# Performance work log

Measured on AMD Instinct MI355X. Metric: run time of the kernel, lower is better.

The kernel has to match this reference:

```python
import jax, jax.numpy as jnp
import numpy as np

DIM = 256
N_EMBED = 1024
COMMITMENT_COST = 0.25


def setup_inputs() -> dict:
    key = jax.random.key(0)
    k1, k2 = jax.random.split(key)
    z = jax.random.normal(k1, (16, 256, 64, 64), dtype=jnp.float32)
    # nn.Embedding weight initialized uniform(-1/n_embed, 1/n_embed)
    embed = jax.random.uniform(k2, (N_EMBED, DIM), dtype=jnp.float32,
                               minval=-1.0 / N_EMBED, maxval=1.0 / N_EMBED)
    return {"z": z, "embed": embed}


def reference(z, embed):
    sg = jax.lax.stop_gradient
    # NCHW -> NHWC, flatten spatial+batch to tokens
    zp = jnp.transpose(z, (0, 2, 3, 1))            # [B,H,W,C]
    zf = zp.reshape(-1, DIM)                        # [N, C]
    # squared euclidean distances via expansion: |z|^2 + |e|^2 - 2 z.e
    d = (jnp.sum(zf * zf, axis=1, keepdims=True)
         + jnp.sum(embed * embed, axis=1)
         - 2.0 * zf @ embed.T)                      # [N, K]
    idx = jnp.argmin(d, axis=1)                     # [N]
    min_encodings = jax.nn.one_hot(idx, N_EMBED, dtype=zf.dtype)  # [N, K]
    # direct gather == one-hot @ embed (same math, one HBM pass)
    z_q = embed[idx].reshape(zp.shape)              # [B,H,W,C]
    loss = (jnp.mean((sg(z_q) - zp) ** 2)
            + COMMITMENT_COST * jnp.mean((z_q - sg(zp)) ** 2))
    # straight-through estimator
    z_q_st = zp + sg(z_q - zp)
    e_mean = jnp.mean(min_encodings, axis=0)
    perplexity = jnp.exp(-jnp.sum(e_mean * jnp.log(e_mean + 1e-10)))
    z_q_out = jnp.transpose(z_q_st, (0, 3, 1, 2))   # back to NCHW
    return (loss, z_q_out, perplexity, min_encodings, idx[:, None])
```

## Files before the change

### kernel.cpp

```cpp
#include <hip/hip_runtime.h>
#include <math.h>

#define DIM    256
#define K_EMB  1024
#define HW     4096
#define CHW    1048576
#define N_TOK  65536
#define NELEM  16777216

#define OUT_LOSS 0
#define OUT_ZQ   1
#define OUT_PERP 16777217
#define OUT_MENC 16777218LL
#define OUT_IDX  83886082

#define TAU  1.5e-4f
#define CAND_CAP 16

#define TAIL_ROW0  65407
#define EH_OFF     66976770LL

typedef short short8  __attribute__((ext_vector_type(8)));
typedef float floatx4 __attribute__((ext_vector_type(4)));
typedef float floatx2 __attribute__((ext_vector_type(2)));

__device__ __forceinline__ unsigned short f2bf(float f) {
    unsigned int u = __float_as_uint(f);
    return (unsigned short)((u + 0x7FFFu + ((u >> 16) & 1u)) >> 16);
}
__device__ __forceinline__ float bf2f(unsigned short h) {
    return __uint_as_float(((unsigned int)h) << 16);
}

__device__ __forceinline__ float np_pair128(const float* p) {
    float r[8];
    #pragma unroll
    for (int j = 0; j < 8; ++j) r[j] = p[j];
    for (int i = 8; i < 128; i += 8)
        #pragma unroll
        for (int j = 0; j < 8; ++j) r[j] = __fadd_rn(r[j], p[i + j]);
    return __fadd_rn(__fadd_rn(__fadd_rn(r[0], r[1]), __fadd_rn(r[2], r[3])),
                     __fadd_rn(__fadd_rn(r[4], r[5]), __fadd_rn(r[6], r[7])));
}
__device__ __forceinline__ float np_pair256(const float* p) {
    return __fadd_rn(np_pair128(p), np_pair128(p + 128));
}

__device__ __forceinline__ void build_frags(const float* __restrict__ zp, int quad, short8* a) {
    #pragma unroll
    for (int kc = 0; kc < 8; ++kc) {
        short8 vh, vl;
        #pragma unroll
        for (int u = 0; u < 8; ++u) {
            float v = __builtin_nontemporal_load(zp + (size_t)(kc * 32 + quad * 8 + u) * HW);
            unsigned short h = f2bf(v);
            vh[u] = (short)h;
            vl[u] = (short)f2bf(v - bf2f(h));
        }
        a[kc]     = vh;
        a[8 + kc] = vl;
    }
}

__global__ void t2_np_kernel(const float* __restrict__ embed, float* __restrict__ t2,
                             unsigned short* __restrict__ Eh) {
    int k = blockIdx.x * 256 + threadIdx.x;
    if (k >= K_EMB) return;
    const float* e = embed + (size_t)k * DIM;
    float p[256];
    for (int c = 0; c < DIM; c += 4) {
        float4 v = *(const float4*)(e + c);
        p[c]     = __fmul_rn(v.x, v.x);
        p[c + 1] = __fmul_rn(v.y, v.y);
        p[c + 2] = __fmul_rn(v.z, v.z);
        p[c + 3] = __fmul_rn(v.w, v.w);
    }
    t2[k] = np_pair256(p);
    unsigned short* dst = Eh + (size_t)k * DIM;
    for (int c0 = 0; c0 < DIM; c0 += 8) {
        short8 vh;
        #pragma unroll
        for (int u = 0; u < 8; ++u) vh[u] = (short)f2bf(e[c0 + u]);
        *(short8*)(dst + c0) = vh;
    }
}

__launch_bounds__(256, 4)
__global__ void vq_mfma(const float* __restrict__ z,
                        const float* __restrict__ embed,
                        const unsigned short* __restrict__ Eh,
                        const float* __restrict__ t2g,
                        float* __restrict__ out,
                        unsigned int* __restrict__ counts,
                        float* __restrict__ loss_sum) {
    __shared__ unsigned short lds_b[32 * 264];
    __shared__ float t2_lds[K_EMB];
    __shared__ int midx[64];
    __shared__ unsigned short clist[64][CAND_CAP];
    __shared__ int ccnt[64];
    __shared__ int flist[64];
    __shared__ int fn;
    __shared__ float pp4[4][256];

    const int tid  = threadIdx.x;
    const int lane = tid & 63;
    const int wv   = tid >> 6;
    const int l15  = lane & 15;
    const int quad = lane >> 4;
    const int m0   = blockIdx.x * 64;

    for (int i = tid; i < K_EMB; i += 256) t2_lds[i] = t2g[i];
    if (tid < 64) ccnt[tid] = 0;
    if (tid == 0) fn = 0;

    short8 a[16];
    {
        const int n = m0 + wv * 16 + l15;
        build_frags(z + (size_t)(n >> 12) * CHW + (n & 4095), quad, a);
    }

    float bs[4], ss[4], tb[4]; int bk[4];
    #pragma unroll
    for (int r = 0; r < 4; ++r) { bs[r] = 3.4e38f; ss[r] = 3.4e38f; tb[r] = 3.4e38f; bk[r] = 0; }

    const int srow = tid >> 3;
    const int scol = (tid & 7) * 32;

    for (int it = 0; it < 32; ++it) {
        const int n0 = it * 32;
        __syncthreads();
        {
            const short8* g = (const short8*)(Eh + (size_t)(n0 + srow) * 256 + scol);
            short8* l = (short8*)(lds_b + srow * 264 + scol);
            short8 v0 = g[0], v1 = g[1], v2 = g[2], v3 = g[3];
            l[0] = v0; l[1] = v1; l[2] = v2; l[3] = v3;
        }
        __syncthreads();
        floatx4 acc0 = {0.f, 0.f, 0.f, 0.f};
        floatx4 acc1 = {0.f, 0.f, 0.f, 0.f};
        #pragma unroll
        for (int kc = 0; kc < 8; ++kc) {
            short8 b0 = *(const short8*)(lds_b + l15 * 264 + kc * 32 + quad * 8);
            short8 b1 = *(const short8*)(lds_b + (16 + l15) * 264 + kc * 32 + quad * 8);
            acc0 = __builtin_amdgcn_mfma_f32_16x16x32_bf16(a[kc],     b0, acc0, 0, 0, 0);
            acc1 = __builtin_amdgcn_mfma_f32_16x16x32_bf16(a[kc],     b1, acc1, 0, 0, 0);
            acc0 = __builtin_amdgcn_mfma_f32_16x16x32_bf16(a[8 + kc], b0, acc0, 0, 0, 0);
            acc1 = __builtin_amdgcn_mfma_f32_16x16x32_bf16(a[8 + kc], b1, acc1, 0, 0, 0);
        }
        float t20 = t2_lds[n0 + l15];
        float t21 = t2_lds[n0 + 16 + l15];
        #pragma unroll
        for (int r = 0; r < 4; ++r) {
            const int trow = wv * 16 + quad * 4 + r;
            float s0 = fmaf(-2.0f, acc0[r], t20);
            if (s0 < bs[r]) { ss[r] = bs[r]; bs[r] = s0; bk[r] = n0 + l15; }
            else if (s0 < ss[r]) ss[r] = s0;
            float s1 = fmaf(-2.0f, acc1[r], t21);
            if (s1 < bs[r]) { ss[r] = bs[r]; bs[r] = s1; bk[r] = n0 + 16 + l15; }
            else if (s1 < ss[r]) ss[r] = s1;

            float m01 = fminf(s0, s1);
            #pragma unroll
            for (int mo = 1; mo < 16; mo <<= 1) m01 = fminf(m01, __shfl_xor(m01, mo, 64));
            tb[r] = fminf(tb[r], m01);
            const float thr = tb[r] + TAU;
            if (s0 <= thr) {
                int pos = atomicAdd(&ccnt[trow], 1);
                if (pos < CAND_CAP) clist[trow][pos] = (unsigned short)(n0 + l15);
            }
            if (s1 <= thr) {
                int pos = atomicAdd(&ccnt[trow], 1);
                if (pos < CAND_CAP) clist[trow][pos] = (unsigned short)(n0 + 16 + l15);
            }
        }
    }

    #pragma unroll
    for (int r = 0; r < 4; ++r) {
        for (int mo = 1; mo < 16; mo <<= 1) {
            float obs = __shfl_xor(bs[r], mo, 64);
            float oss = __shfl_xor(ss[r], mo, 64);
            int   obk = __shfl_xor(bk[r], mo, 64);
            if (obs < bs[r] || (obs == bs[r] && obk < bk[r])) {
                ss[r] = fminf(bs[r], oss); bs[r] = obs; bk[r] = obk;
            } else {
                ss[r] = fminf(ss[r], obs);
            }
        }
        if (l15 == 0) {
            int tl = wv * 16 + quad * 4 + r;
            midx[tl] = bk[r];
            if (ss[r] - bs[r] < TAU) {
                int p = atomicAdd(&fn, 1);
                flist[p] = tl;
            }
        }
    }
    __syncthreads();

    const int nfb = fn;
    for (int f = wv; f < nfb; f += 4) {
        const int tl = flist[f];
        const int n  = m0 + tl;
        const int cnt = ccnt[tl];

        const float* zt = z + (size_t)(n >> 12) * CHW + (n & 4095);
        double zd[4];
        #pragma unroll
        for (int u = 0; u < 4; ++u) {
            float v = zt[(size_t)(lane + u * 64) * HW];
            zd[u] = (double)v;
            pp4[wv][lane + u * 64] = __fmul_rn(v, v);
        }
        __asm__ volatile("s_waitcnt lgkmcnt(0)" ::: "memory");
        float rj = 0.0f;
        if (lane < 16) {
            int jj = lane & 7, half = lane >> 3;
            const float* p = &pp4[wv][half * 128 + jj];
            rj = p[0];
            #pragma unroll
            for (int ii = 1; ii < 16; ++ii) rj = __fadd_rn(rj, p[ii * 8]);
        }
        float v0 = __shfl(rj, 0, 64), v1 = __shfl(rj, 1, 64), v2 = __shfl(rj, 2, 64), v3 = __shfl(rj, 3, 64);
        float v4 = __shfl(rj, 4, 64), v5 = __shfl(rj, 5, 64), v6 = __shfl(rj, 6, 64), v7 = __shfl(rj, 7, 64);
        float h0 = __fadd_rn(__fadd_rn(__fadd_rn(v0, v1), __fadd_rn(v2, v3)),
                             __fadd_rn(__fadd_rn(v4, v5), __fadd_rn(v6, v7)));
        v0 = __shfl(rj,  8, 64); v1 = __shfl(rj,  9, 64); v2 = __shfl(rj, 10, 64); v3 = __shfl(rj, 11, 64);
        v4 = __shfl(rj, 12, 64); v5 = __shfl(rj, 13, 64); v6 = __shfl(rj, 14, 64); v7 = __shfl(rj, 15, 64);
        float h1 = __fadd_rn(__fadd_rn(__fadd_rn(v0, v1), __fadd_rn(v2, v3)),
                             __fadd_rn(__fadd_rn(v4, v5), __fadd_rn(v6, v7)));
        const float t1 = __fadd_rn(h0, h1);

        float bd = 3.4e38f; int bkk = 1 << 30;
        if (cnt <= CAND_CAP) {
            for (int ci = 0; ci < cnt; ++ci) {
                int k = clist[tl][ci];
                const float* e = embed + (size_t)k * DIM;
                double s = 0.0;
                #pragma unroll
                for (int u = 0; u < 4; ++u) s = fma(zd[u], (double)e[lane + u * 64], s);
                for (int mo = 1; mo < 64; mo <<= 1) s += __shfl_xor(s, mo, 64);
                float rho = (float)s;
                float d = __fadd_rn(__fadd_rn(t1, t2_lds[k]), -__fmul_rn(2.0f, rho));
                if (d < bd || (d == bd && k < bkk)) { bd = d; bkk = k; }
            }
        } else {
            for (int k = 0; k < K_EMB; ++k) {
                const float* e = embed + (size_t)k * DIM;
                double s = 0.0;
                #pragma unroll
                for (int u = 0; u < 4; ++u) s = fma(zd[u], (double)e[lane + u * 64], s);
                for (int mo = 1; mo < 64; mo <<= 1) s += __shfl_xor(s, mo, 64);
                float rho = (float)s;
                float d = __fadd_rn(__fadd_rn(t1, t2_lds[k]), -__fmul_rn(2.0f, rho));
                if (d < bd) { bd = d; bkk = k; }
            }
        }
        if (lane == 0) midx[tl] = bkk;
    }
    __syncthreads();

    if (tid < 64) {
        const int id = midx[tid];
        out[OUT_IDX + m0 + tid] = (float)id;
        atomicAdd(&counts[id], 1u);
    }

    {
        const int n   = m0 + wv * 16 + l15;
        const int myk = midx[wv * 16 + l15];
        const float* erow = embed + (size_t)myk * DIM;
        float* zqp = out + OUT_ZQ + (size_t)(n >> 12) * CHW + (n & 4095);
        float lsum = 0.0f;
        #pragma unroll
        for (int kc = 0; kc < 8; ++kc) {
            const int c0 = kc * 32 + quad * 8;
            float4 e0 = *(const float4*)(erow + c0);
            float4 e1 = *(const float4*)(erow + c0 + 4);
            float ev[8] = {e0.x, e0.y, e0.z, e0.w, e1.x, e1.y, e1.z, e1.w};
            #pragma unroll
            for (int u = 0; u < 8; ++u) {
                float vv = __fadd_rn(bf2f((unsigned short)a[kc][u]),
                                     bf2f((unsigned short)a[8 + kc][u]));
                float dz = ev[u] - vv;
                lsum = fmaf(dz, dz, lsum);
                __builtin_nontemporal_store(ev[u], zqp + (size_t)(c0 + u) * HW);
            }
        }
        #pragma unroll
        for (int off = 32; off > 0; off >>= 1) lsum += __shfl_down(lsum, off, 64);
        if (lane == 0) atomicAdd(loss_sum, lsum);
    }

    #pragma unroll 1
    for (int j = 0; j < 64; ++j) {
        if (m0 + j >= TAIL_ROW0) break;
        const int id = midx[j];
        floatx2* dst = (floatx2*)(out + OUT_MENC + (size_t)(m0 + j) * K_EMB);
        int c0 = tid * 2;
        floatx2 v;  v.x  = (c0 == id)       ? 1.0f : 0.0f;  v.y  = (c0 + 1 == id)  ? 1.0f : 0.0f;
        __builtin_nontemporal_store(v, dst + tid);
        int c1 = c0 + 512;
        floatx2 w2; w2.x = (c1 == id)       ? 1.0f : 0.0f;  w2.y = (c1 + 1 == id)  ? 1.0f : 0.0f;
        __builtin_nontemporal_store(w2, dst + 256 + tid);
    }
}

__global__ void menc_tail(float* __restrict__ out) {
    const int row = TAIL_ROW0 + blockIdx.x;
    const int id  = (int)out[OUT_IDX + row];
    floatx2* dst = (floatx2*)(out + OUT_MENC + (size_t)row * K_EMB);
    int c0 = threadIdx.x * 2;
    floatx2 v;  v.x  = (c0 == id)      ? 1.0f : 0.0f;  v.y  = (c0 + 1 == id) ? 1.0f : 0.0f;
    dst[threadIdx.x] = v;
    int c1 = c0 + 512;
    floatx2 w;  w.x  = (c1 == id)      ? 1.0f : 0.0f;  w.y  = (c1 + 1 == id) ? 1.0f : 0.0f;
    dst[256 + threadIdx.x] = w;
}

__global__ void finalize_kernel(const unsigned int* __restrict__ counts,
                                const float* __restrict__ loss_sum,
                                float* __restrict__ out) {
    __shared__ float red[256];
    int tid = threadIdx.x;
    float hsum = 0.0f;
    for (int k = tid; k < K_EMB; k += 256) {
        float p = (float)counts[k] * (1.0f / 65536.0f);
        hsum += p * logf(p + 1e-10f);
    }
    red[tid] = hsum;
    __syncthreads();
    for (int s = 128; s > 0; s >>= 1) {
        if (tid < s) red[tid] += red[tid + s];
        __syncthreads();
    }
    if (tid == 0) {
        out[OUT_PERP] = expf(-red[0]);
        out[OUT_LOSS] = loss_sum[0] * 1.25f * (1.0f / (float)NELEM);
    }
}

extern "C" void kernel_launch(void* const* d_in, const int* in_sizes, int n_in,
                              void* d_out, int out_size, void* d_ws, size_t ws_size,
                              hipStream_t stream) {
    const float* z     = (const float*)d_in[0];
    const float* embed = (const float*)d_in[1];
    float* out = (float*)d_out;

    unsigned int* counts = (unsigned int*)d_ws;
    float* loss_sum      = (float*)((char*)d_ws + 4096);
    float* t2g           = (float*)((char*)d_ws + 8192);

    float* scr = out + OUT_MENC;
    unsigned short* Eh = (unsigned short*)(scr + EH_OFF);

    (void)hipMemsetAsync(d_ws, 0, 4104, stream);
    t2_np_kernel   <<<dim3(4),    dim3(256), 0, stream>>>(embed, t2g, Eh);
    vq_mfma        <<<dim3(1024), dim3(256), 0, stream>>>(z, embed, Eh, t2g, out, counts, loss_sum);
    menc_tail      <<<dim3(129),  dim3(256), 0, stream>>>(out);
    finalize_kernel<<<dim3(1),    dim3(256), 0, stream>>>(counts, loss_sum, out);
}
```

Baseline: 726.5 us.

## Track top-2 candidates per lane and coalesce z_q store with z reload

Replaces the per-tile shuffle-min plus LDS atomic candidate list with per-lane best/second-best tracking and a near-tie counter. The packed pairs go to shared memory for exact fp64 refinement, and a full scan runs when any lane sees more than two close candidates. The z_q/loss epilogue now has each wave cover 64 channels with lanes mapped to tokens. This makes the z re-read and z_q stores coalesced along spatial positions, instead of rebuilding z from the bf16 split fragments. The z loads in build_frags also drop the nontemporal hint so the reload can hit cache, at the cost of a second read of z.

```diff
diff --git a/kernel.cpp b/kernel.cpp
--- a/kernel.cpp
+++ b/kernel.cpp
@@ -15,7 +15,6 @@
 #define OUT_IDX  83886082
 
 #define TAU  1.5e-4f
-#define CAND_CAP 16
 
 #define TAIL_ROW0  65407
 #define EH_OFF     66976770LL
@@ -52,7 +51,7 @@
         short8 vh, vl;
         #pragma unroll
         for (int u = 0; u < 8; ++u) {
-            float v = __builtin_nontemporal_load(zp + (size_t)(kc * 32 + quad * 8 + u) * HW);
+            float v = zp[(size_t)(kc * 32 + quad * 8 + u) * HW];
             unsigned short h = f2bf(v);
             vh[u] = (short)h;
             vl[u] = (short)f2bf(v - bf2f(h));
@@ -96,8 +95,8 @@
     __shared__ unsigned short lds_b[32 * 264];
     __shared__ float t2_lds[K_EMB];
     __shared__ int midx[64];
-    __shared__ unsigned short clist[64][CAND_CAP];
-    __shared__ int ccnt[64];
+    __shared__ unsigned int cand[64][16];
+    __shared__ int ovfl[64];
     __shared__ int flist[64];
     __shared__ int fn;
     __shared__ float pp4[4][256];
@@ -110,7 +109,6 @@
     const int m0   = blockIdx.x * 64;
 
     for (int i = tid; i < K_EMB; i += 256) t2_lds[i] = t2g[i];
-    if (tid < 64) ccnt[tid] = 0;
     if (tid == 0) fn = 0;
 
     short8 a[16];
@@ -119,9 +117,9 @@
         build_frags(z + (size_t)(n >> 12) * CHW + (n & 4095), quad, a);
     }
 
-    float bs[4], ss[4], tb[4]; int bk[4];
+    float bs[4], ss[4]; int bk[4], sk[4], cl[4];
     #pragma unroll
-    for (int r = 0; r < 4; ++r) { bs[r] = 3.4e38f; ss[r] = 3.4e38f; tb[r] = 3.4e38f; bk[r] = 0; }
+    for (int r = 0; r < 4; ++r) { bs[r] = 3.4e38f; ss[r] = 3.4e38f; bk[r] = 0; sk[r] = 0; cl[r] = 0; }
 
     const int srow = tid >> 3;
     const int scol = (tid & 7) * 32;
@@ -151,32 +149,27 @@
         float t21 = t2_lds[n0 + 16 + l15];
         #pragma unroll
         for (int r = 0; r < 4; ++r) {
-            const int trow = wv * 16 + quad * 4 + r;
             float s0 = fmaf(-2.0f, acc0[r], t20);
-            if (s0 < bs[r]) { ss[r] = bs[r]; bs[r] = s0; bk[r] = n0 + l15; }
-            else if (s0 < ss[r]) ss[r] = s0;
+            if (s0 < bs[r]) { ss[r] = bs[r]; sk[r] = bk[r]; bs[r] = s0; bk[r] = n0 + l15; }
+            else if (s0 < ss[r]) { ss[r] = s0; sk[r] = n0 + l15; }
+            cl[r] += (s0 <= bs[r] + TAU) ? 1 : 0;
             float s1 = fmaf(-2.0f, acc1[r], t21);
-            if (s1 < bs[r]) { ss[r] = bs[r]; bs[r] = s1; bk[r] = n0 + 16 + l15; }
-            else if (s1 < ss[r]) ss[r] = s1;
-
-            float m01 = fminf(s0, s1);
-            #pragma unroll
-            for (int mo = 1; mo < 16; mo <<= 1) m01 = fminf(m01, __shfl_xor(m01, mo, 64));
-            tb[r] = fminf(tb[r], m01);
-            const float thr = tb[r] + TAU;
-            if (s0 <= thr) {
-                int pos = atomicAdd(&ccnt[trow], 1);
-                if (pos < CAND_CAP) clist[trow][pos] = (unsigned short)(n0 + l15);
-            }
-            if (s1 <= thr) {
-                int pos = atomicAdd(&ccnt[trow], 1);
-                if (pos < CAND_CAP) clist[trow][pos] = (unsigned short)(n0 + 16 + l15);
-            }
+            if (s1 < bs[r]) { ss[r] = bs[r]; sk[r] = bk[r]; bs[r] = s1; bk[r] = n0 + 16 + l15; }
+            else if (s1 < ss[r]) { ss[r] = s1; sk[r] = n0 + 16 + l15; }
+            cl[r] += (s1 <= bs[r] + TAU) ? 1 : 0;
         }
     }
 
     #pragma unroll
     for (int r = 0; r < 4; ++r) {
+        const int trow = wv * 16 + quad * 4 + r;
+        cand[trow][l15] = ((unsigned int)sk[r] << 16) | (unsigned int)bk[r];
+        int mcl = cl[r];
+        #pragma unroll
+        for (int mo = 1; mo < 16; mo <<= 1) {
+            int o = __shfl_xor(mcl, mo, 64);
+            mcl = (o > mcl) ? o : mcl;
+        }
         for (int mo = 1; mo < 16; mo <<= 1) {
             float obs = __shfl_xor(bs[r], mo, 64);
             float oss = __shfl_xor(ss[r], mo, 64);
@@ -188,11 +181,11 @@
             }
         }
         if (l15 == 0) {
-            int tl = wv * 16 + quad * 4 + r;
-            midx[tl] = bk[r];
+            midx[trow] = bk[r];
+            ovfl[trow] = (mcl > 2) ? 1 : 0;
             if (ss[r] - bs[r] < TAU) {
                 int p = atomicAdd(&fn, 1);
-                flist[p] = tl;
+                flist[p] = trow;
             }
         }
     }
@@ -202,7 +195,6 @@
     for (int f = wv; f < nfb; f += 4) {
         const int tl = flist[f];
         const int n  = m0 + tl;
-        const int cnt = ccnt[tl];
 
         const float* zt = z + (size_t)(n >> 12) * CHW + (n & 4095);
         double zd[4];
@@ -232,17 +224,21 @@
         const float t1 = __fadd_rn(h0, h1);
 
         float bd = 3.4e38f; int bkk = 1 << 30;
-        if (cnt <= CAND_CAP) {
-            for (int ci = 0; ci < cnt; ++ci) {
-                int k = clist[tl][ci];
-                const float* e = embed + (size_t)k * DIM;
-                double s = 0.0;
+        if (!ovfl[tl]) {
+            for (int cp = 0; cp < 16; ++cp) {
+                unsigned int pk = cand[tl][cp];
                 #pragma unroll
-                for (int u = 0; u < 4; ++u) s = fma(zd[u], (double)e[lane + u * 64], s);
-                for (int mo = 1; mo < 64; mo <<= 1) s += __shfl_xor(s, mo, 64);
-                float rho = (float)s;
-                float d = __fadd_rn(__fadd_rn(t1, t2_lds[k]), -__fmul_rn(2.0f, rho));
-                if (d < bd || (d == bd && k < bkk)) { bd = d; bkk = k; }
+                for (int hf = 0; hf < 2; ++hf) {
+                    int k = hf ? (int)(pk >> 16) : (int)(pk & 0xFFFFu);
+                    const float* e = embed + (size_t)k * DIM;
+                    double s = 0.0;
+                    #pragma unroll
+                    for (int u = 0; u < 4; ++u) s = fma(zd[u], (double)e[lane + u * 64], s);
+                    for (int mo = 1; mo < 64; mo <<= 1) s += __shfl_xor(s, mo, 64);
+                    float rho = (float)s;
+                    float d = __fadd_rn(__fadd_rn(t1, t2_lds[k]), -__fmul_rn(2.0f, rho));
+                    if (d < bd || (d == bd && k < bkk)) { bd = d; bkk = k; }
+                }
             }
         } else {
             for (int k = 0; k < K_EMB; ++k) {
@@ -267,25 +263,21 @@
     }
 
     {
-        const int n   = m0 + wv * 16 + l15;
-        const int myk = midx[wv * 16 + l15];
-        const float* erow = embed + (size_t)myk * DIM;
-        float* zqp = out + OUT_ZQ + (size_t)(n >> 12) * CHW + (n & 4095);
+        const int b    = m0 >> 12;
+        const int rem0 = m0 & 4095;
+        const float* zbase  = z   + (size_t)b * CHW + rem0;
+        float*       zqbase = out + OUT_ZQ + (size_t)b * CHW + rem0;
+        const int myk = midx[lane];
+        const size_t erow = (size_t)myk * DIM;
         float lsum = 0.0f;
-        #pragma unroll
-        for (int kc = 0; kc < 8; ++kc) {
-            const int c0 = kc * 32 + quad * 8;
-            float4 e0 = *(const float4*)(erow + c0);
-            float4 e1 = *(const float4*)(erow + c0 + 4);
-            float ev[8] = {e0.x, e0.y, e0.z, e0.w, e1.x, e1.y, e1.z, e1.w};
-            #pragma unroll
-            for (int u = 0; u < 8; ++u) {
-                float vv = __fadd_rn(bf2f((unsigned short)a[kc][u]),
-                                     bf2f((unsigned short)a[8 + kc][u]));
-                float dz = ev[u] - vv;
-                lsum = fmaf(dz, dz, lsum);
-                __builtin_nontemporal_store(ev[u], zqp + (size_t)(c0 + u) * HW);
-            }
+        #pragma unroll 4
+        for (int cc = 0; cc < 64; ++cc) {
+            const int c = wv * 64 + cc;
+            float e  = embed[erow + c];
+            float zv = zbase[(size_t)c * HW + lane];
+            float dz = e - zv;
+            lsum = fmaf(dz, dz, lsum);
+            __builtin_nontemporal_store(e, zqbase + (size_t)c * HW + lane);
         }
         #pragma unroll
         for (int off = 32; off > 0; off >>= 1) lsum += __shfl_down(lsum, off, 64);
```

Result: slower. 1.291 ms (+77.7%).
